# Kernel optimization log

Hardware: AMD Instinct MI355X
Metric: run time of the kernel (lower is better)

## Reference

```python
import jax, jax.numpy as jnp
import numpy as np

B, V, L, H = 4, 1024, 2048, 2048
TEMP = 1.0
EPS = 1e-12


def _l2norm(x):
    # F.normalize(x, dim=-1): x / max(||x||, eps)
    n = jnp.linalg.norm(x, axis=-1, keepdims=True)
    return x / jnp.maximum(n, EPS)


def setup_inputs() -> dict:
    key = jax.random.key(0)
    k1, k2, k3, k4 = jax.random.split(key, 4)
    std = H ** (-0.5)
    return {
        "vision_features": jax.random.normal(k1, (B, V, H), dtype=jnp.float32),
        "language_features": jax.random.normal(k2, (B, L, H), dtype=jnp.float32),
        "W_vl": jax.random.normal(k3, (H, 2 * H), dtype=jnp.float32) * std,  # vision_language_gate.weight
        "W_lv": jax.random.normal(k4, (H, 2 * H), dtype=jnp.float32) * std,  # language_vision_gate.weight
    }


def reference(vision_features, language_features, W_vl, W_lv):
    b, vsl, h = vision_features.shape
    lsl = language_features.shape[1]
    max_len = max(vsl, lsl)

    # zero-pad both modalities to max_len along seq dim
    vis_p = jnp.pad(vision_features, ((0, 0), (0, max_len - vsl), (0, 0)))
    lang_p = jnp.pad(language_features, ((0, 0), (0, max_len - lsl), (0, 0)))

    # cosine-similarity attention (fp32 softmax)
    scores = jnp.einsum("bvh,blh->bvl", _l2norm(vis_p), _l2norm(lang_p)) / TEMP
    weights = jax.nn.softmax(scores.astype(jnp.float32), axis=-1).astype(vision_features.dtype)
    fused = jnp.einsum("bvl,blh->bvh", weights, lang_p)  # [b, max_len, h]

    # mean pooling over padded sequences (includes zero padding, as in torch)
    vis_avg = jnp.mean(vis_p, axis=1, keepdims=True)    # [b,1,h]
    lang_avg = jnp.mean(lang_p, axis=1, keepdims=True)  # [b,1,h]

    # sigmoid gates: cat([avg.expand, other], -1) @ W.T
    v2l = jnp.concatenate([jnp.broadcast_to(vis_avg, lang_p.shape), lang_p], axis=-1)
    vl_gate = jax.nn.sigmoid(jnp.einsum("bld,hd->blh", v2l, W_vl))
    l2v = jnp.concatenate([jnp.broadcast_to(lang_avg, vis_p.shape), vis_p], axis=-1)
    lv_gate = jax.nn.sigmoid(jnp.einsum("bvd,hd->bvh", l2v, W_lv))

    vision_output = vision_features + fused[:, :vsl, :] * lv_gate[:, :vsl, :]
    language_output = language_features + fused[:, :lsl, :] * vl_gate[:, :lsl, :]
    return fused[:, :max_len, :], vision_output, language_output
```

## Files before the change

### kernel.cpp

```cpp
#include <hip/hip_runtime.h>

#define H_ 2048

typedef __attribute__((ext_vector_type(8))) short short8;
typedef __attribute__((ext_vector_type(4))) float f32x4;
typedef __attribute__((ext_vector_type(4))) unsigned int u32x4;
typedef __attribute__((ext_vector_type(4))) unsigned short u16x4;

__device__ __forceinline__ unsigned short f2bf(float f) {
  unsigned int u = __builtin_bit_cast(unsigned int, f);
  u += 0x7FFFu + ((u >> 16) & 1u);
  return (unsigned short)(u >> 16);
}
__device__ __forceinline__ float bf2f(unsigned short h) {
  unsigned int u = ((unsigned int)h) << 16;
  return __builtin_bit_cast(float, u);
}
__device__ __forceinline__ unsigned int pk2(float a, float b) {
  return (unsigned int)f2bf(a) | ((unsigned int)f2bf(b) << 16);
}

#define GLDS16(gp, lp)                                                 \
  __builtin_amdgcn_global_load_lds(                                    \
      (const __attribute__((address_space(1))) void*)(gp),             \
      (__attribute__((address_space(3))) void*)(lp), 16, 0, 0)

__global__ __launch_bounds__(256) void prep_rows(
    const float* __restrict__ in, long sIn,
    unsigned short* __restrict__ outBf, long sOut,
    float* __restrict__ rnorm, int validRows) {
  const int tid = threadIdx.x;
  const int r = blockIdx.x, b = blockIdx.y;
  unsigned short* orow = outBf + (long)b * sOut + (long)r * H_ + tid * 8;
  if (r >= validRows) {
    *(u32x4*)orow = (u32x4){0u, 0u, 0u, 0u};
    if (tid == 0) rnorm[b * H_ + r] = 0.f;
    return;
  }
  const float* row = in + (long)b * sIn + (long)r * H_ + tid * 8;
  f32x4 x0 = *(const f32x4*)row;
  f32x4 x1 = *(const f32x4*)(row + 4);
  float ss = x0[0]*x0[0] + x0[1]*x0[1] + x0[2]*x0[2] + x0[3]*x0[3]
           + x1[0]*x1[0] + x1[1]*x1[1] + x1[2]*x1[2] + x1[3]*x1[3];
#pragma unroll
  for (int o = 32; o; o >>= 1) ss += __shfl_xor(ss, o, 64);
  __shared__ float red[4];
  if ((tid & 63) == 0) red[tid >> 6] = ss;
  __syncthreads();
  if (tid == 0) {
    float tot = red[0] + red[1] + red[2] + red[3];
    rnorm[b * H_ + r] = 1.f / fmaxf(sqrtf(tot), 1e-12f);
  }
  u32x4 o;
  o[0] = pk2(x0[0], x0[1]); o[1] = pk2(x0[2], x0[3]);
  o[2] = pk2(x1[0], x1[1]); o[3] = pk2(x1[2], x1[3]);
  *(u32x4*)orow = o;
}

__global__ __launch_bounds__(256) void col_sum_part_bf(
    const unsigned short* __restrict__ visBf,
    const unsigned short* __restrict__ langBf, float* __restrict__ part) {
  const int h = blockIdx.x * 256 + threadIdx.x;
  const int y = blockIdx.y;
  const int which = blockIdx.z & 1;
  const int b = blockIdx.z >> 1;
  const long sP = 2048L * 2048;
  const unsigned short* p =
      (which ? langBf : visBf) + (long)b * sP + (long)(y * 256) * H_ + h;
  float s = 0.f;
#pragma unroll 4
  for (int i = 0; i < 256; ++i) s += bf2f(p[(long)i * H_]);
  part[(((long)which * 4 + b) * 8 + y) * H_ + h] = s;
}

__global__ __launch_bounds__(256) void col_sum_final(
    const float* __restrict__ part, float* __restrict__ vavg,
    float* __restrict__ lavg) {
  const int h = blockIdx.x * 256 + threadIdx.x;
  const int b = blockIdx.y;
  const int which = blockIdx.z;
  const float* p = part + (((long)which * 4 + b) * 8) * H_ + h;
  float s = 0.f;
#pragma unroll
  for (int y = 0; y < 8; ++y) s += p[y * H_];
  (which ? lavg : vavg)[b * H_ + h] = s * (1.f / 2048.f);
}

__global__ __launch_bounds__(256) void bias_gemv(
    const float* __restrict__ W, const float* __restrict__ avg,
    float* __restrict__ bias) {
  const int lane = threadIdx.x & 63;
  const int wv = threadIdx.x >> 6;
  const int h = blockIdx.x * 4 + wv;
  const float* wrow = W + (long)h * 4096;
  float a0 = 0.f, a1 = 0.f, a2 = 0.f, a3 = 0.f;
#pragma unroll
  for (int i = 0; i < 8; ++i) {
    const int d = i * 256 + lane * 4;
    f32x4 w4 = *(const f32x4*)(wrow + d);
    f32x4 v0 = *(const f32x4*)(avg + 0 * H_ + d);
    f32x4 v1 = *(const f32x4*)(avg + 1 * H_ + d);
    f32x4 v2 = *(const f32x4*)(avg + 2 * H_ + d);
    f32x4 v3 = *(const f32x4*)(avg + 3 * H_ + d);
    a0 += w4[0]*v0[0] + w4[1]*v0[1] + w4[2]*v0[2] + w4[3]*v0[3];
    a1 += w4[0]*v1[0] + w4[1]*v1[1] + w4[2]*v1[2] + w4[3]*v1[3];
    a2 += w4[0]*v2[0] + w4[1]*v2[1] + w4[2]*v2[2] + w4[3]*v2[3];
    a3 += w4[0]*v3[0] + w4[1]*v3[1] + w4[2]*v3[2] + w4[3]*v3[3];
  }
#pragma unroll
  for (int o = 32; o; o >>= 1) {
    a0 += __shfl_xor(a0, o, 64);
    a1 += __shfl_xor(a1, o, 64);
    a2 += __shfl_xor(a2, o, 64);
    a3 += __shfl_xor(a3, o, 64);
  }
  if (lane == 0) {
    bias[0 * H_ + h] = a0; bias[1 * H_ + h] = a1;
    bias[2 * H_ + h] = a2; bias[3 * H_ + h] = a3;
  }
}

__global__ __launch_bounds__(256) void transpose_bf(
    const unsigned short* __restrict__ in, unsigned short* __restrict__ out) {
  __shared__ unsigned short tle[64][72];
  const int b = blockIdx.z;
  const int l0 = blockIdx.y * 64, h0 = blockIdx.x * 64;
  const unsigned short* inb = in + (long)b * (2048L * 2048);
  unsigned short* outb = out + (long)b * (2048L * 2048);
#pragma unroll
  for (int i = 0; i < 16; ++i) {
    const int idx = i * 256 + threadIdx.x;
    const int r = idx >> 6, c = idx & 63;
    tle[r][c] = inb[(long)(l0 + r) * H_ + h0 + c];
  }
  __syncthreads();
#pragma unroll
  for (int i = 0; i < 16; ++i) {
    const int idx = i * 256 + threadIdx.x;
    const int r = idx >> 6, c = idx & 63;
    outb[(long)(h0 + r) * H_ + l0 + c] = tle[c][r];
  }
}

__global__ __launch_bounds__(256) void extract_whi(
    const float* __restrict__ Wvl, const float* __restrict__ Wlv,
    unsigned short* __restrict__ WvlHi, unsigned short* __restrict__ WlvHi) {
  const int h = blockIdx.x;
  const int which = blockIdx.y;
  const float* src = (which ? Wlv : Wvl) + (long)h * 4096 + 2048 + threadIdx.x * 8;
  unsigned short* dst = (which ? WlvHi : WvlHi) + (long)h * H_ + threadIdx.x * 8;
  f32x4 x0 = *(const f32x4*)src;
  f32x4 x1 = *(const f32x4*)(src + 4);
  u32x4 o;
  o[0] = pk2(x0[0], x0[1]); o[1] = pk2(x0[2], x0[3]);
  o[2] = pk2(x1[0], x1[1]); o[3] = pk2(x1[2], x1[3]);
  *(u32x4*)dst = o;
}

__global__ __launch_bounds__(256) void bcast_fused(
    const float* __restrict__ lavg, float* __restrict__ fused) {
  const int b = blockIdx.y;
  const long r = 1024 + blockIdx.x;
  const int c = threadIdx.x * 8;
  f32x4 v0 = *(const f32x4*)(lavg + b * H_ + c);
  f32x4 v1 = *(const f32x4*)(lavg + b * H_ + c + 4);
  float* dst = fused + (long)b * (2048L * 2048) + r * H_ + c;
  *(f32x4*)dst = v0;
  *(f32x4*)(dst + 4) = v1;
}

__global__ __launch_bounds__(256) void softmax_rows(unsigned short* __restrict__ S) {
  const int tid = threadIdx.x;
  const int lane = tid & 63, wv = tid >> 6;
  const int b = blockIdx.x >> 10;
  const int r = blockIdx.x & 1023;
  unsigned short* rowp =
      S + (long)b * (2048L * 2048) + (long)r * H_ + tid * 8;
  u32x4 raw = *(const u32x4*)rowp;
  float v[8];
#pragma unroll
  for (int i = 0; i < 4; ++i) {
    v[2 * i]     = bf2f((unsigned short)(raw[i] & 0xFFFFu));
    v[2 * i + 1] = bf2f((unsigned short)(raw[i] >> 16));
  }
  float mx = v[0];
#pragma unroll
  for (int i = 1; i < 8; ++i) mx = fmaxf(mx, v[i]);
#pragma unroll
  for (int o = 32; o; o >>= 1) mx = fmaxf(mx, __shfl_xor(mx, o, 64));
  __shared__ float red[4];
  if (lane == 0) red[wv] = mx;
  __syncthreads();
  const float MX = fmaxf(fmaxf(red[0], red[1]), fmaxf(red[2], red[3]));
  float p[8], s = 0.f;
#pragma unroll
  for (int i = 0; i < 8; ++i) { p[i] = __expf(v[i] - MX); s += p[i]; }
#pragma unroll
  for (int o = 32; o; o >>= 1) s += __shfl_xor(s, o, 64);
  __syncthreads();
  if (lane == 0) red[wv] = s;
  __syncthreads();
  const float inv = 1.f / (red[0] + red[1] + red[2] + red[3]);
  u32x4 o;
#pragma unroll
  for (int i = 0; i < 4; ++i) o[i] = pk2(p[2 * i] * inv, p[2 * i + 1] * inv);
  *(u32x4*)rowp = o;
}

struct EpArgs {
  unsigned short* Sout; const float* rv; const float* rl;
  float* Fout;
  const unsigned short* residBf; const float* fusedIn;
  const float* bias; float* Oout;
  long sResid, sFused, sOut;
  const unsigned short* A2; const unsigned short* B2;
  const unsigned short* residBf2; const float* bias2; float* Oout2;
  long sResid2, sOut2;
};

#define BAR_ asm volatile("s_barrier" ::: "memory")
#define WAITV_(n) asm volatile("s_waitcnt vmcnt(" #n ")" ::: "memory")
#define LGKM0_ asm volatile("s_waitcnt lgkmcnt(0)" ::: "memory")
#define SB_ __builtin_amdgcn_sched_barrier(0)

template <int MODE>
__global__ __launch_bounds__(256, 2) void gemm_nt(
    const unsigned short* __restrict__ A, long sA,
    const unsigned short* __restrict__ B, long sB, EpArgs ep) {
  __shared__ unsigned short LDS[32768];

  const int tid = threadIdx.x;
  const int lane = tid & 63;
  const int wave = tid >> 6;

  const int gx = gridDim.x, gy = gridDim.y;
  const int nwg = gx * gy * gridDim.z;
  const int lin = blockIdx.x + gx * (blockIdx.y + gy * blockIdx.z);
  const int swz = (lin & 7) * (nwg >> 3) + (lin >> 3);
  const int bx = swz % gx;
  const int rest = swz / gx;
  const int by = rest % gy;
  const int b = rest / gy;
  const int bn = bx << 7;

  int bm;
  const unsigned short* Ab;
  const unsigned short* Bb;
  const unsigned short* RbBf = nullptr;
  const float *Fb = nullptr, *biasb = nullptr;
  float* Ob = nullptr;
  if (MODE == 3) {
    const bool second = (by >= 16);
    bm = (second ? by - 16 : by) << 7;
    Ab = (second ? ep.A2 : A) + (long)b * sA;
    Bb = second ? ep.B2 : B;
    RbBf = (second ? ep.residBf2 : ep.residBf) +
           (long)b * (second ? ep.sResid2 : ep.sResid);
    Ob = (second ? ep.Oout2 : ep.Oout) +
         (long)b * (second ? ep.sOut2 : ep.sOut);
    biasb = (second ? ep.bias2 : ep.bias) + b * H_;
    Fb = ep.fusedIn + (long)b * ep.sFused;
  } else {
    bm = by << 7;
    Ab = A + (long)b * sA;
    Bb = B + (long)b * sB;
  }

  const int srow = tid >> 3;
  const int colOff = (((tid & 7) ^ (srow & 7)) << 3);
  const unsigned short* gA = Ab + (long)(bm + srow) * H_ + colOff;
  const unsigned short* gB = Bb + (long)(bn + srow) * H_ + colOff;
  const int ldst = wave * 512;

#define STAGE_(kt, P)                                               \
  do {                                                              \
    const unsigned short* a_ = gA + (kt) * 64;                      \
    const unsigned short* b_ = gB + (kt) * 64;                      \
    GLDS16(a_,           &LDS[(P) * 16384 + 0     + ldst]);         \
    GLDS16(a_ + 32 * H_, &LDS[(P) * 16384 + 2048  + ldst]);         \
    GLDS16(a_ + 64 * H_, &LDS[(P) * 16384 + 4096  + ldst]);         \
    GLDS16(a_ + 96 * H_, &LDS[(P) * 16384 + 6144  + ldst]);         \
    GLDS16(b_,           &LDS[(P) * 16384 + 8192  + ldst]);         \
    GLDS16(b_ + 32 * H_, &LDS[(P) * 16384 + 10240 + ldst]);         \
    GLDS16(b_ + 64 * H_, &LDS[(P) * 16384 + 12288 + ldst]);         \
    GLDS16(b_ + 96 * H_, &LDS[(P) * 16384 + 14336 + ldst]);         \
  } while (0)

  const int row16 = lane & 15;
  const int kg = lane >> 4;
  const int wr = (wave >> 1) << 6;
  const int wc = (wave & 1) << 6;
  const int x0 = ((kg ^ (row16 & 7)) << 4);
  const int x1 = (((4 + kg) ^ (row16 & 7)) << 4);

  const unsigned bAk0 = (unsigned)(unsigned long long)(
      __attribute__((address_space(3))) const void*)LDS +
      (unsigned)((wr + row16) * 128 + x0);
  const unsigned bAk1 = bAk0 + (unsigned)(x1 - x0);
  const unsigned bBk0 = (unsigned)(unsigned long long)(
      __attribute__((address_space(3))) const void*)LDS +
      (unsigned)(16384 + (wc + row16) * 128 + x0);
  const unsigned bBk1 = bBk0 + (unsigned)(x1 - x0);

#define DSRD_(dst, base, off) \
  asm volatile("ds_read_b128 %0, %1 offset:" #off : "=v"(dst) : "v"(base))

  f32x4 acc[4][4];
#pragma unroll
  for (int m = 0; m < 4; ++m)
#pragma unroll
    for (int n = 0; n < 4; ++n) acc[m][n] = (f32x4){0.f, 0.f, 0.f, 0.f};
  short8 aF[4][2], bF[4][2];

#define RDALL_P0                                           \
  do {                                                     \
    DSRD_(aF[0][0], bAk0, 0);    DSRD_(aF[1][0], bAk0, 2048);  \
    DSRD_(aF[2][0], bAk0, 4096); DSRD_(aF[3][0], bAk0, 6144);  \
    DSRD_(aF[0][1], bAk1, 0);    DSRD_(aF[1][1], bAk1, 2048);  \
    DSRD_(aF[2][1], bAk1, 4096); DSRD_(aF[3][1], bAk1, 6144);  \
    DSRD_(bF[0][0], bBk0, 0);    DSRD_(bF[1][0], bBk0, 2048);  \
    DSRD_(bF[2][0], bBk0, 4096); DSRD_(bF[3][0], bBk0, 6144);  \
    DSRD_(bF[0][1], bBk1, 0);    DSRD_(bF[1][1], bBk1, 2048);  \
    DSRD_(bF[2][1], bBk1, 4096); DSRD_(bF[3][1], bBk1, 6144);  \
  } while (0)
#define RDALL_P1                                                   \
  do {                                                             \
    DSRD_(aF[0][0], bAk0, 32768); DSRD_(aF[1][0], bAk0, 34816);   \
    DSRD_(aF[2][0], bAk0, 36864); DSRD_(aF[3][0], bAk0, 38912);   \
    DSRD_(aF[0][1], bAk1, 32768); DSRD_(aF[1][1], bAk1, 34816);   \
    DSRD_(aF[2][1], bAk1, 36864); DSRD_(aF[3][1], bAk1, 38912);   \
    DSRD_(bF[0][0], bBk0, 32768); DSRD_(bF[1][0], bBk0, 34816);   \
    DSRD_(bF[2][0], bBk0, 36864); DSRD_(bF[3][0], bBk0, 38912);   \
    DSRD_(bF[0][1], bBk1, 32768); DSRD_(bF[1][1], bBk1, 34816);   \
    DSRD_(bF[2][1], bBk1, 36864); DSRD_(bF[3][1], bBk1, 38912);   \
  } while (0)

#define MFMA32_                                                             \
  do {                                                                      \
    __builtin_amdgcn_s_setprio(1);                                          \
    _Pragma("unroll") for (int ks_ = 0; ks_ < 2; ++ks_)                     \
    _Pragma("unroll") for (int m_ = 0; m_ < 4; ++m_)                        \
    _Pragma("unroll") for (int n_ = 0; n_ < 4; ++n_)                        \
        acc[m_][n_] = __builtin_amdgcn_mfma_f32_16x16x32_bf16(              \
            aF[m_][ks_], bF[n_][ks_], acc[m_][n_], 0, 0, 0);                \
    __builtin_amdgcn_s_setprio(0);                                          \
  } while (0)

  STAGE_(0, 0); STAGE_(1, 1);
  WAITV_(8);
  BAR_;

  for (int tt = 0; tt < 15; ++tt) {
    const int t2 = tt * 2;
    RDALL_P0; LGKM0_; SB_;
    BAR_;
    STAGE_(t2 + 2, 0);
    WAITV_(8);
    BAR_;
    MFMA32_;
    RDALL_P1; LGKM0_; SB_;
    BAR_;
    STAGE_(t2 + 3, 1);
    WAITV_(8);
    BAR_;
    MFMA32_;
  }
  RDALL_P0; LGKM0_; SB_;
  BAR_;
  WAITV_(0);
  BAR_;
  MFMA32_;
  RDALL_P1; LGKM0_; SB_;
  MFMA32_;

  const int cr0 = bm + wr + kg * 4;
  const int cc0 = bn + wc + row16;

  if (MODE == 0) {
    float rvv[4][4], rlv[4];
#pragma unroll
    for (int m = 0; m < 4; ++m)
#pragma unroll
      for (int j = 0; j < 4; ++j) rvv[m][j] = ep.rv[b * H_ + cr0 + m * 16 + j];
#pragma unroll
    for (int n = 0; n < 4; ++n) rlv[n] = ep.rl[b * H_ + cc0 + n * 16];
    unsigned short* Sb = ep.Sout + (long)b * (H_ * (long)H_);
#pragma unroll
    for (int m = 0; m < 4; ++m)
#pragma unroll
      for (int n = 0; n < 4; ++n)
#pragma unroll
        for (int j = 0; j < 4; ++j) {
          const long idx = (long)(cr0 + m * 16 + j) * H_ + cc0 + n * 16;
          Sb[idx] = f2bf(acc[m][n][j] * rvv[m][j] * rlv[n]);
        }
  } else {
    float* LF = (float*)LDS;
    __syncthreads();
    const int lwr = wr + kg * 4;
    const int lwc = wc + row16;
#pragma unroll
    for (int m = 0; m < 4; ++m)
#pragma unroll
      for (int n = 0; n < 4; ++n)
#pragma unroll
        for (int j = 0; j < 4; ++j) {
          const int r = lwr + m * 16 + j;
          const int c = lwc + n * 16;
          LF[r * 128 + ((c + 4 * r) & 127)] = acc[m][n][j];
        }
    __syncthreads();
    const int r8 = tid >> 5;
    const int c4 = (tid & 31) * 4;
    if (MODE == 1) {
      float* Fo = ep.Fout + (long)b * (H_ * (long)H_);
#pragma unroll
      for (int it = 0; it < 16; ++it) {
        const int r = it * 8 + r8;
        f32x4 v = *(const f32x4*)&LF[r * 128 + ((c4 + 4 * r) & 127)];
        *(f32x4*)&Fo[(long)(bm + r) * H_ + bn + c4] = v;
      }
    } else {
      const f32x4 bvv = *(const f32x4*)&biasb[bn + c4];
#pragma unroll
      for (int it = 0; it < 16; ++it) {
        const int r = it * 8 + r8;
        f32x4 v = *(const f32x4*)&LF[r * 128 + ((c4 + 4 * r) & 127)];
        const long off = (long)(bm + r) * H_ + bn + c4;
        const f32x4 fv = *(const f32x4*)&Fb[off];
        const u16x4 rb4 = *(const u16x4*)&RbBf[off];
        f32x4 o;
#pragma unroll
        for (int k = 0; k < 4; ++k) {
          const float x = v[k] + bvv[k];
          const float g = 1.f / (1.f + __expf(-x));
          o[k] = bf2f(rb4[k]) + fv[k] * g;
        }
        *(f32x4*)&Ob[off] = o;
      }
    }
  }
#undef STAGE_
#undef DSRD_
#undef RDALL_P0
#undef RDALL_P1
#undef MFMA32_
}

extern "C" void kernel_launch(void* const* d_in, const int* in_sizes, int n_in,
                              void* d_out, int out_size, void* d_ws,
                              size_t ws_size, hipStream_t stream) {
  (void)in_sizes; (void)n_in; (void)out_size; (void)ws_size;
  const float* vis = (const float*)d_in[0];
  const float* lang = (const float*)d_in[1];
  const float* Wvl = (const float*)d_in[2];
  const float* Wlv = (const float*)d_in[3];

  float* out = (float*)d_out;
  float* fused = out;
  float* vis_out = out + 16777216;
  float* lang_out = out + 25165824;
  unsigned short* S = (unsigned short*)lang_out;
  unsigned short* langT = (unsigned short*)vis_out;

  char* w = (char*)d_ws;
  unsigned short* vis_bf = (unsigned short*)w;
  unsigned short* lang_bf = (unsigned short*)(w + 33554432);
  unsigned short* WvlHi = (unsigned short*)(w + 67108864);
  unsigned short* WlvHi = (unsigned short*)(w + 75497472);
  float* rv      = (float*)(w + 83886080);
  float* rl      = (float*)(w + 83918848);
  float* vavg    = (float*)(w + 83951616);
  float* lavg    = (float*)(w + 83984384);
  float* bias_vl = (float*)(w + 84017152);
  float* bias_lv = (float*)(w + 84049920);
  float* part    = (float*)(w + 84082688);

  const long sV = 1024L * 2048, sL = 2048L * 2048, sP = 2048L * 2048;

  prep_rows<<<dim3(2048, 4), 256, 0, stream>>>(vis, sV, vis_bf, sP, rv, 1024);
  prep_rows<<<dim3(2048, 4), 256, 0, stream>>>(lang, sL, lang_bf, sP, rl, 2048);
  col_sum_part_bf<<<dim3(8, 8, 8), 256, 0, stream>>>(vis_bf, lang_bf, part);
  col_sum_final<<<dim3(8, 4, 2), 256, 0, stream>>>(part, vavg, lavg);
  bias_gemv<<<512, 256, 0, stream>>>(Wvl, vavg, bias_vl);
  bias_gemv<<<512, 256, 0, stream>>>(Wlv, lavg, bias_lv);
  transpose_bf<<<dim3(32, 32, 4), 256, 0, stream>>>(lang_bf, langT);
  extract_whi<<<dim3(2048, 2), 256, 0, stream>>>(Wvl, Wlv, WvlHi, WlvHi);
  bcast_fused<<<dim3(1024, 4), 256, 0, stream>>>(lavg, fused);

  EpArgs e1 = {};
  e1.Sout = S; e1.rv = rv; e1.rl = rl;
  gemm_nt<0><<<dim3(16, 8, 4), 256, 0, stream>>>(vis_bf, sP, lang_bf, sP, e1);

  softmax_rows<<<4096, 256, 0, stream>>>(S);

  EpArgs e2 = {};
  e2.Fout = fused;
  gemm_nt<1><<<dim3(16, 8, 4), 256, 0, stream>>>(S, sP, langT, sP, e2);

  EpArgs e34 = {};
  e34.residBf = lang_bf; e34.sResid = sP;
  e34.fusedIn = fused; e34.sFused = sP;
  e34.bias = bias_vl; e34.Oout = lang_out; e34.sOut = sL;
  e34.A2 = vis_bf; e34.B2 = WlvHi;
  e34.residBf2 = vis_bf; e34.sResid2 = sP;
  e34.bias2 = bias_lv; e34.Oout2 = vis_out; e34.sOut2 = sV;
  gemm_nt<3><<<dim3(16, 24, 4), 256, 0, stream>>>(lang_bf, sP, WvlHi, 0L, e34);
}
```

Before: 293.3 us.

## Load B operand fragments directly from global into registers, bypassing LDS

```diff
diff --git a/kernel.cpp b/kernel.cpp
--- a/kernel.cpp
+++ b/kernel.cpp
@@ -269,21 +269,15 @@
   const int srow = tid >> 3;
   const int colOff = (((tid & 7) ^ (srow & 7)) << 3);
   const unsigned short* gA = Ab + (long)(bm + srow) * H_ + colOff;
-  const unsigned short* gB = Bb + (long)(bn + srow) * H_ + colOff;
   const int ldst = wave * 512;
 
 #define STAGE_(kt, P)                                               \
   do {                                                              \
     const unsigned short* a_ = gA + (kt) * 64;                      \
-    const unsigned short* b_ = gB + (kt) * 64;                      \
-    GLDS16(a_,           &LDS[(P) * 16384 + 0     + ldst]);         \
-    GLDS16(a_ + 32 * H_, &LDS[(P) * 16384 + 2048  + ldst]);         \
-    GLDS16(a_ + 64 * H_, &LDS[(P) * 16384 + 4096  + ldst]);         \
-    GLDS16(a_ + 96 * H_, &LDS[(P) * 16384 + 6144  + ldst]);         \
-    GLDS16(b_,           &LDS[(P) * 16384 + 8192  + ldst]);         \
-    GLDS16(b_ + 32 * H_, &LDS[(P) * 16384 + 10240 + ldst]);         \
-    GLDS16(b_ + 64 * H_, &LDS[(P) * 16384 + 12288 + ldst]);         \
-    GLDS16(b_ + 96 * H_, &LDS[(P) * 16384 + 14336 + ldst]);         \
+    GLDS16(a_,           &LDS[(P) * 8192 + 0    + ldst]);           \
+    GLDS16(a_ + 32 * H_, &LDS[(P) * 8192 + 2048 + ldst]);           \
+    GLDS16(a_ + 64 * H_, &LDS[(P) * 8192 + 4096 + ldst]);           \
+    GLDS16(a_ + 96 * H_, &LDS[(P) * 8192 + 6144 + ldst]);           \
   } while (0)
 
   const int row16 = lane & 15;
@@ -297,81 +291,93 @@
       __attribute__((address_space(3))) const void*)LDS +
       (unsigned)((wr + row16) * 128 + x0);
   const unsigned bAk1 = bAk0 + (unsigned)(x1 - x0);
-  const unsigned bBk0 = (unsigned)(unsigned long long)(
-      __attribute__((address_space(3))) const void*)LDS +
-      (unsigned)(16384 + (wc + row16) * 128 + x0);
-  const unsigned bBk1 = bBk0 + (unsigned)(x1 - x0);
+
+  unsigned long long a0 =
+      (unsigned long long)(Bb + (long)(bn + wc + row16) * H_ + kg * 8);
+  unsigned long long a1 = a0 + (unsigned long long)(16L * H_ * 2);
+  unsigned long long a2 = a0 + (unsigned long long)(32L * H_ * 2);
+  unsigned long long a3 = a0 + (unsigned long long)(48L * H_ * 2);
 
 #define DSRD_(dst, base, off) \
   asm volatile("ds_read_b128 %0, %1 offset:" #off : "=v"(dst) : "v"(base))
+#define GLB16_(dst, addr, off)                                   \
+  asm volatile("global_load_dwordx4 %0, %1, off offset:" #off    \
+               : "=v"(dst) : "v"(addr))
 
   f32x4 acc[4][4];
 #pragma unroll
   for (int m = 0; m < 4; ++m)
 #pragma unroll
     for (int n = 0; n < 4; ++n) acc[m][n] = (f32x4){0.f, 0.f, 0.f, 0.f};
-  short8 aF[4][2], bF[4][2];
-
-#define RDALL_P0                                           \
-  do {                                                     \
-    DSRD_(aF[0][0], bAk0, 0);    DSRD_(aF[1][0], bAk0, 2048);  \
-    DSRD_(aF[2][0], bAk0, 4096); DSRD_(aF[3][0], bAk0, 6144);  \
-    DSRD_(aF[0][1], bAk1, 0);    DSRD_(aF[1][1], bAk1, 2048);  \
-    DSRD_(aF[2][1], bAk1, 4096); DSRD_(aF[3][1], bAk1, 6144);  \
-    DSRD_(bF[0][0], bBk0, 0);    DSRD_(bF[1][0], bBk0, 2048);  \
-    DSRD_(bF[2][0], bBk0, 4096); DSRD_(bF[3][0], bBk0, 6144);  \
-    DSRD_(bF[0][1], bBk1, 0);    DSRD_(bF[1][1], bBk1, 2048);  \
-    DSRD_(bF[2][1], bBk1, 4096); DSRD_(bF[3][1], bBk1, 6144);  \
+  short8 aF[4][2], bfC[4][2], bfN[4][2];
+
+#define BLOAD_(bf)                                     \
+  do {                                                 \
+    GLB16_(bf[0][0], a0, 0); GLB16_(bf[0][1], a0, 64); \
+    GLB16_(bf[1][0], a1, 0); GLB16_(bf[1][1], a1, 64); \
+    GLB16_(bf[2][0], a2, 0); GLB16_(bf[2][1], a2, 64); \
+    GLB16_(bf[3][0], a3, 0); GLB16_(bf[3][1], a3, 64); \
+    a0 += 128; a1 += 128; a2 += 128; a3 += 128;        \
   } while (0)
-#define RDALL_P1                                                   \
-  do {                                                             \
-    DSRD_(aF[0][0], bAk0, 32768); DSRD_(aF[1][0], bAk0, 34816);   \
-    DSRD_(aF[2][0], bAk0, 36864); DSRD_(aF[3][0], bAk0, 38912);   \
-    DSRD_(aF[0][1], bAk1, 32768); DSRD_(aF[1][1], bAk1, 34816);   \
-    DSRD_(aF[2][1], bAk1, 36864); DSRD_(aF[3][1], bAk1, 38912);   \
-    DSRD_(bF[0][0], bBk0, 32768); DSRD_(bF[1][0], bBk0, 34816);   \
-    DSRD_(bF[2][0], bBk0, 36864); DSRD_(bF[3][0], bBk0, 38912);   \
-    DSRD_(bF[0][1], bBk1, 32768); DSRD_(bF[1][1], bBk1, 34816);   \
-    DSRD_(bF[2][1], bBk1, 36864); DSRD_(bF[3][1], bBk1, 38912);   \
+
+#define RDA_P0                                                \
+  do {                                                        \
+    DSRD_(aF[0][0], bAk0, 0);    DSRD_(aF[1][0], bAk0, 2048); \
+    DSRD_(aF[2][0], bAk0, 4096); DSRD_(aF[3][0], bAk0, 6144); \
+    DSRD_(aF[0][1], bAk1, 0);    DSRD_(aF[1][1], bAk1, 2048); \
+    DSRD_(aF[2][1], bAk1, 4096); DSRD_(aF[3][1], bAk1, 6144); \
   } while (0)
-
-#define MFMA32_                                                             \
+#define RDA_P1                                                    \
+  do {                                                            \
+    DSRD_(aF[0][0], bAk0, 16384); DSRD_(aF[1][0], bAk0, 18432);   \
+    DSRD_(aF[2][0], bAk0, 20480); DSRD_(aF[3][0], bAk0, 22528);   \
+    DSRD_(aF[0][1], bAk1, 16384); DSRD_(aF[1][1], bAk1, 18432);   \
+    DSRD_(aF[2][1], bAk1, 20480); DSRD_(aF[3][1], bAk1, 22528);   \
+  } while (0)
+
+#define MFMA32_(BF)                                                         \
   do {                                                                      \
     __builtin_amdgcn_s_setprio(1);                                          \
     _Pragma("unroll") for (int ks_ = 0; ks_ < 2; ++ks_)                     \
     _Pragma("unroll") for (int m_ = 0; m_ < 4; ++m_)                        \
     _Pragma("unroll") for (int n_ = 0; n_ < 4; ++n_)                        \
         acc[m_][n_] = __builtin_amdgcn_mfma_f32_16x16x32_bf16(              \
-            aF[m_][ks_], bF[n_][ks_], acc[m_][n_], 0, 0, 0);                \
+            aF[m_][ks_], BF[n_][ks_], acc[m_][n_], 0, 0, 0);                \
     __builtin_amdgcn_s_setprio(0);                                          \
   } while (0)
 
-  STAGE_(0, 0); STAGE_(1, 1);
-  WAITV_(8);
-  BAR_;
-
-  for (int tt = 0; tt < 15; ++tt) {
-    const int t2 = tt * 2;
-    RDALL_P0; LGKM0_; SB_;
+  STAGE_(0, 0);
+  BLOAD_(bfC);
+  STAGE_(1, 1);
+  WAITV_(4); SB_;
+  BAR_; SB_;
+
+  for (int i = 0; i < 15; ++i) {
+    const int t2 = i * 2;
+    RDA_P0; LGKM0_; SB_;
     BAR_;
     STAGE_(t2 + 2, 0);
-    WAITV_(8);
-    BAR_;
-    MFMA32_;
-    RDALL_P1; LGKM0_; SB_;
+    BLOAD_(bfN);
+    WAITV_(12); SB_;
+    BAR_; SB_;
+    MFMA32_(bfC);
+    RDA_P1; LGKM0_; SB_;
     BAR_;
     STAGE_(t2 + 3, 1);
-    WAITV_(8);
-    BAR_;
-    MFMA32_;
-  }
-  RDALL_P0; LGKM0_; SB_;
+    BLOAD_(bfC);
+    WAITV_(12); SB_;
+    BAR_; SB_;
+    MFMA32_(bfN);
+  }
+  RDA_P0; LGKM0_; SB_;
   BAR_;
-  WAITV_(0);
-  BAR_;
-  MFMA32_;
-  RDALL_P1; LGKM0_; SB_;
-  MFMA32_;
+  BLOAD_(bfN);
+  WAITV_(8); SB_;
+  BAR_; SB_;
+  MFMA32_(bfC);
+  RDA_P1; LGKM0_; SB_;
+  WAITV_(0); SB_;
+  MFMA32_(bfN);
 
   const int cr0 = bm + wr + kg * 4;
   const int cc0 = bn + wc + row16;
@@ -442,8 +448,10 @@
   }
 #undef STAGE_
 #undef DSRD_
-#undef RDALL_P0
-#undef RDALL_P1
+#undef GLB16_
+#undef BLOAD_
+#undef RDA_P0
+#undef RDA_P1
 #undef MFMA32_
 }
 
```

After: 463.2 us. 57.9% more time.
